# Optimization experiments

Hardware: AMD Instinct MI355X
Metric: run time of the kernel (lower is better)

Reference implementation:

```python
import jax, jax.numpy as jnp
import numpy as np

B, D, L, E, H = 8192, 1024, 256, 16, 400

def setup_inputs() -> dict:
    key = jax.random.key(0)
    ks = jax.random.split(key, 6)
    s1 = 1.0 / np.sqrt(D)
    s2 = 1.0 / np.sqrt(H)
    return {
        "x": jax.random.normal(ks[0], (B, D), dtype=jnp.float32),
        "angle_idx": jax.random.randint(ks[1], (B,), 0, E, dtype=jnp.int64),
        "W1": jax.random.uniform(ks[2], (E, D, H), jnp.float32, -s1, s1),
        "b1": jax.random.uniform(ks[3], (E, H), jnp.float32, -s1, s1),
        "W2": jax.random.uniform(ks[4], (E, H, 2 * L), jnp.float32, -s2, s2),
        "b2": jax.random.uniform(ks[5], (E, 2 * L), jnp.float32, -s2, s2),
    }

def reference(x, angle_idx, W1, b1, W2, b2):
    # Dense all-experts compute, then per-sample select (jit-friendly MoE dispatch).
    # h1: [E, B, H]
    h1 = jax.nn.relu(jnp.einsum('bd,edh->ebh', x, W1) + b1[:, None, :])
    # h: [E, B, 2L]
    h = jnp.einsum('ebh,ehk->ebk', h1, W2) + b2[:, None, :]
    sel = h[angle_idx, jnp.arange(x.shape[0])]  # [B, 2L], each row from its routed expert
    half = sel.shape[1] // 2
    z_mu, z_logvar = sel[:, :half], sel[:, half:]
    return (z_mu, z_logvar)
```

## Files before the change

kernel.cpp:

```cpp
#include <hip/hip_runtime.h>
#include <hip/hip_bf16.h>
#include <cstdint>
#include <cstddef>

#define B_N 8192
#define D_K 1024
#define H_N 400
#define HP  416
#define K2_N 512
#define E_N 16
#define L_N 256
#define TM 64
#define PAD_ROWS (B_N + E_N * TM)
#define NTILES (PAD_ROWS / TM)

typedef short bf16x8 __attribute__((ext_vector_type(8)));
typedef float f32x4 __attribute__((ext_vector_type(4)));

#define GLDS(gp, lp) __builtin_amdgcn_global_load_lds( \
    (const __attribute__((address_space(1))) unsigned int*)(gp), \
    (__attribute__((address_space(3))) unsigned int*)(lp), 16, 0, 0)

static __device__ __forceinline__ unsigned short f2bf(float f) {
  union { float f; unsigned int u; } c; c.f = f;
  unsigned int u = c.u + 0x7fffu + ((c.u >> 16) & 1u);
  return (unsigned short)(u >> 16);
}
static __device__ __forceinline__ unsigned int pkbf(float a, float b) {
  union { __hip_bfloat162 v; unsigned int u; } c;
  c.v = __float22bfloat162_rn(make_float2(a, b));
  return c.u;
}

__global__ __launch_bounds__(256) void prep_kernel(const float* __restrict__ W1,
                                                   const float* __restrict__ W2,
                                                   const float* __restrict__ x,
                                                   const int* __restrict__ idx,
                                                   unsigned short* __restrict__ Wt1,
                                                   unsigned short* __restrict__ Wt2,
                                                   unsigned short* __restrict__ xc,
                                                   int* __restrict__ off_al,
                                                   int* __restrict__ cnt_al,
                                                   int* __restrict__ order) {
  const int bid = blockIdx.x;
  const int t = threadIdx.x;
  if (bid < 2688) {
    __shared__ unsigned short Ls[64][72];
    const float* S; unsigned short* Dt; int K, N, Kd, Nd, k0, n0;
    if (bid < 1792) {
      int e = bid / 112, r = bid % 112;
      k0 = (r % 16) * 64; n0 = (r / 16) * 64;
      S = W1 + (size_t)e * D_K * H_N; Dt = Wt1 + (size_t)e * HP * D_K;
      K = D_K; N = H_N; Kd = D_K; Nd = HP;
    } else {
      int t2 = bid - 1792; int e = t2 / 56, r = t2 % 56;
      k0 = (r % 7) * 64; n0 = (r / 7) * 64;
      S = W2 + (size_t)e * H_N * K2_N; Dt = Wt2 + (size_t)e * K2_N * HP;
      K = H_N; N = K2_N; Kd = HP; Nd = K2_N;
    }
    const int kk = t >> 4;
    const int nn = (t & 15) * 4;
    float4 v[4];
#pragma unroll
    for (int p = 0; p < 4; ++p) {
      int k = k0 + p * 16 + kk;
      int n = n0 + nn;
      v[p] = make_float4(0.f, 0.f, 0.f, 0.f);
      if (k < K && n + 3 < N) v[p] = *(const float4*)(S + (size_t)k * N + n);
    }
#pragma unroll
    for (int p = 0; p < 4; ++p) {
      Ls[nn + 0][p * 16 + kk] = f2bf(v[p].x);
      Ls[nn + 1][p * 16 + kk] = f2bf(v[p].y);
      Ls[nn + 2][p * 16 + kk] = f2bf(v[p].z);
      Ls[nn + 3][p * 16 + kk] = f2bf(v[p].w);
    }
    __syncthreads();
    const int n2 = t >> 3;
    const int ch = t & 7;
#pragma unroll
    for (int p = 0; p < 2; ++p) {
      int n = n0 + p * 32 + n2;
      int k = k0 + ch * 8;
      if (n < Nd && k < Kd)
        *(uint4*)(Dt + (size_t)n * Kd + k) = *(const uint4*)&Ls[p * 32 + n2][ch * 8];
    }
  } else if (bid < 3200) {
    const int xb = bid - 2688;
    const float* S = x + (size_t)xb * 16 * D_K;
    unsigned short* Dp = xc + (size_t)xb * 16 * D_K;
#pragma unroll
    for (int i = 0; i < 16; ++i) {
      float4 v = *(const float4*)(S + i * D_K + t * 4);
      uint2 o; o.x = pkbf(v.x, v.y); o.y = pkbf(v.z, v.w);
      *(uint2*)(Dp + i * D_K + t * 4) = o;
    }
  } else {
    const int hb = bid - 3200;
    __shared__ int totL[E_N], preL[E_N], offsL[E_N], curL[E_N];
    if (t < E_N) { totL[t] = 0; preL[t] = 0; }
    __syncthreads();
    const int lim = hb * 256;
    for (int i = t; i < B_N; i += 256) {
      const int e0 = idx[i];
      atomicAdd(&totL[e0], 1);
      if (i < lim) atomicAdd(&preL[e0], 1);
    }
    __syncthreads();
    if (t == 0) {
      int acc = 0;
      for (int e = 0; e < E_N; ++e) {
        offsL[e] = acc;
        if (hb == 0) off_al[e] = acc;
        acc += ((totL[e] + TM - 1) / TM) * TM;
      }
      if (hb == 0) off_al[E_N] = acc;
    }
    __syncthreads();
    if (t < E_N) {
      curL[t] = offsL[t] + preL[t];
      if (hb == 0) cnt_al[t] = totL[t];
    }
    __syncthreads();
    const int b = hb * 256 + t;
    const int e = idx[b];
    const int slot = atomicAdd(&curL[e], 1);
    order[slot] = b;
    if (hb == 0) *(uint2*)(xc + (size_t)B_N * D_K + t * 4) = make_uint2(0, 0);
  }
}

static __device__ __forceinline__ void swz_decode(int bx, int by, int& mt, int& nb) {
  const int L = bx + NTILES * by;
  const int vid = (L & 7) * 72 + (L >> 3);
  mt = vid >> 2;
  nb = vid & 3;
}

__global__ __launch_bounds__(256) void gemm1_kernel(const unsigned short* __restrict__ xc,
                                                    const unsigned short* __restrict__ Wt1,
                                                    const float* __restrict__ b1,
                                                    const int* __restrict__ off_al,
                                                    const int* __restrict__ cnt_al,
                                                    const int* __restrict__ order,
                                                    unsigned short* __restrict__ h1buf) {
  __shared__ unsigned short As[2 * 2 * 2048];
  __shared__ unsigned short Bs[2 * 2 * 4096];
  __shared__ int offs[E_N + 1];
  __shared__ int rowidx[TM];
  const int tid = threadIdx.x;
  int mt, nb;
  swz_decode(blockIdx.x, blockIdx.y, mt, nb);
  const int m0 = mt * TM;
  if (tid <= E_N) offs[tid] = off_al[tid];
  __syncthreads();
  if (m0 >= offs[E_N]) return;
  int e = 0;
  while (m0 >= offs[e + 1]) ++e;
  if (tid < TM) {
    const bool valid = (m0 + tid) < (offs[e] + cnt_al[e]);
    rowidx[tid] = valid ? order[m0 + tid] : B_N;
  }
  __syncthreads();
  const unsigned short* Wt1e = Wt1 + (size_t)e * HP * D_K;

  const int l = tid & 63, w = tid >> 6;
  const int r4 = l >> 2;
  const int sg = (r4 ^ (r4 >> 2)) & 3;
  const int g8 = ((l & 3) ^ sg) * 8;
  const int t0 = nb * 8 + 2 * w;
  const bool act0 = (t0 < 25);
  const bool act1 = (t0 + 1 < 25);
  const unsigned short* gA = xc + (size_t)rowidx[16 * w + r4] * D_K + g8;
  const unsigned short* gB0 = Wt1e + (size_t)(t0 * 16 + r4) * D_K + g8;
  const unsigned short* gB1 = gB0 + (size_t)16 * D_K;

  const int ln = l & 15, q = l >> 4;
  const int sr = (ln ^ (ln >> 2)) & 3;
  const int cq = (q ^ sr) * 8;

  f32x4 acc[4][2] = {};

#pragma unroll
  for (int ks = 0; ks < 2; ++ks) {
    GLDS(gA + ks * 32, &As[ks * 2048 + 16 * w * 32]);
    if (act0) GLDS(gB0 + ks * 32, &Bs[ks * 4096 + (2 * w + 0) * 512]);
    if (act1) GLDS(gB1 + ks * 32, &Bs[ks * 4096 + (2 * w + 1) * 512]);
  }

  for (int k0 = 0; k0 < D_K; k0 += 64) {
    const int cur = (k0 >> 6) & 1;
    const int nxt = cur ^ 1;
    __syncthreads();
    if (k0 + 64 < D_K) {
#pragma unroll
      for (int ks = 0; ks < 2; ++ks) {
        const int kg = k0 + 64 + ks * 32;
        GLDS(gA + kg, &As[nxt * 4096 + ks * 2048 + 16 * w * 32]);
        if (act0) GLDS(gB0 + kg, &Bs[nxt * 8192 + ks * 4096 + (2 * w + 0) * 512]);
        if (act1) GLDS(gB1 + kg, &Bs[nxt * 8192 + ks * 4096 + (2 * w + 1) * 512]);
      }
    }
    if (act0) {
#pragma unroll
      for (int ks = 0; ks < 2; ++ks) {
        const unsigned short* Ab = &As[cur * 4096 + ks * 2048];
        const unsigned short* Bb = &Bs[cur * 8192 + ks * 4096];
        bf16x8 af[4];
#pragma unroll
        for (int i = 0; i < 4; ++i)
          af[i] = *(const bf16x8*)&Ab[(16 * i + ln) * 32 + cq];
        bf16x8 b0f = *(const bf16x8*)&Bb[(2 * w + 0) * 512 + ln * 32 + cq];
#pragma unroll
        for (int i = 0; i < 4; ++i)
          acc[i][0] = __builtin_amdgcn_mfma_f32_16x16x32_bf16(b0f, af[i], acc[i][0], 0, 0, 0);
        if (act1) {
          bf16x8 b1f = *(const bf16x8*)&Bb[(2 * w + 1) * 512 + ln * 32 + cq];
#pragma unroll
          for (int i = 0; i < 4; ++i)
            acc[i][1] = __builtin_amdgcn_mfma_f32_16x16x32_bf16(b1f, af[i], acc[i][1], 0, 0, 0);
        }
      }
    }
  }

#pragma unroll
  for (int j = 0; j < 2; ++j) {
    if (j == 0 ? act0 : act1) {
      const int n4 = (t0 + j) * 16 + 4 * q;
      const float4 bv = *(const float4*)&b1[e * H_N + n4];
#pragma unroll
      for (int i = 0; i < 4; ++i) {
        const size_t m = (size_t)(m0 + 16 * i + ln);
        uint2 o;
        o.x = pkbf(fmaxf(acc[i][j][0] + bv.x, 0.f), fmaxf(acc[i][j][1] + bv.y, 0.f));
        o.y = pkbf(fmaxf(acc[i][j][2] + bv.z, 0.f), fmaxf(acc[i][j][3] + bv.w, 0.f));
        *(uint2*)&h1buf[m * HP + n4] = o;
      }
    }
  }
}

__global__ __launch_bounds__(256) void gemm2_kernel(const unsigned short* __restrict__ h1buf,
                                                    const unsigned short* __restrict__ Wt2,
                                                    const float* __restrict__ b2,
                                                    const int* __restrict__ off_al,
                                                    const int* __restrict__ cnt_al,
                                                    const int* __restrict__ order,
                                                    float* __restrict__ out) {
  __shared__ unsigned short As[2 * 2 * 2048];
  __shared__ unsigned short Bs[2 * 2 * 4096];
  __shared__ int offs[E_N + 1];
  __shared__ int rowidx[TM];
  const int tid = threadIdx.x;
  int mt, nb;
  swz_decode(blockIdx.x, blockIdx.y, mt, nb);
  const int m0 = mt * TM;
  if (tid <= E_N) offs[tid] = off_al[tid];
  __syncthreads();
  if (m0 >= offs[E_N]) return;
  int e = 0;
  while (m0 >= offs[e + 1]) ++e;
  if (tid < TM) {
    const bool valid = (m0 + tid) < (offs[e] + cnt_al[e]);
    rowidx[tid] = valid ? order[m0 + tid] : -1;
  }
  __syncthreads();
  const unsigned short* Wt2e = Wt2 + (size_t)e * K2_N * HP;

  const int l = tid & 63, w = tid >> 6;
  const int r4 = l >> 2;
  const int sg = (r4 ^ (r4 >> 2)) & 3;
  const int g8 = ((l & 3) ^ sg) * 8;
  const int t0 = nb * 8 + 2 * w;
  const unsigned short* gA = h1buf + (size_t)(m0 + 16 * w + r4) * HP + g8;
  const unsigned short* gB0 = Wt2e + (size_t)(t0 * 16 + r4) * HP + g8;
  const unsigned short* gB1 = gB0 + (size_t)16 * HP;

  const int ln = l & 15, q = l >> 4;
  const int sr = (ln ^ (ln >> 2)) & 3;
  const int cq = (q ^ sr) * 8;

  f32x4 acc[4][2] = {};

#pragma unroll
  for (int ks = 0; ks < 2; ++ks) {
    GLDS(gA + ks * 32, &As[ks * 2048 + 16 * w * 32]);
    GLDS(gB0 + ks * 32, &Bs[ks * 4096 + (2 * w + 0) * 512]);
    GLDS(gB1 + ks * 32, &Bs[ks * 4096 + (2 * w + 1) * 512]);
  }

  for (int k0 = 0; k0 < HP; k0 += 64) {
    const int cur = (k0 >> 6) & 1;
    const int nxt = cur ^ 1;
    __syncthreads();
#pragma unroll
    for (int ks = 0; ks < 2; ++ks) {
      const int kg = k0 + 64 + ks * 32;
      if (kg < HP) {
        GLDS(gA + kg, &As[nxt * 4096 + ks * 2048 + 16 * w * 32]);
        GLDS(gB0 + kg, &Bs[nxt * 8192 + ks * 4096 + (2 * w + 0) * 512]);
        GLDS(gB1 + kg, &Bs[nxt * 8192 + ks * 4096 + (2 * w + 1) * 512]);
      }
    }
#pragma unroll
    for (int ks = 0; ks < 2; ++ks) {
      if (k0 + ks * 32 < HP) {
        const unsigned short* Ab = &As[cur * 4096 + ks * 2048];
        const unsigned short* Bb = &Bs[cur * 8192 + ks * 4096];
        bf16x8 af[4];
#pragma unroll
        for (int i = 0; i < 4; ++i)
          af[i] = *(const bf16x8*)&Ab[(16 * i + ln) * 32 + cq];
        bf16x8 b0f = *(const bf16x8*)&Bb[(2 * w + 0) * 512 + ln * 32 + cq];
#pragma unroll
        for (int i = 0; i < 4; ++i)
          acc[i][0] = __builtin_amdgcn_mfma_f32_16x16x32_bf16(b0f, af[i], acc[i][0], 0, 0, 0);
        bf16x8 b1f = *(const bf16x8*)&Bb[(2 * w + 1) * 512 + ln * 32 + cq];
#pragma unroll
        for (int i = 0; i < 4; ++i)
          acc[i][1] = __builtin_amdgcn_mfma_f32_16x16x32_bf16(b1f, af[i], acc[i][1], 0, 0, 0);
      }
    }
  }

#pragma unroll
  for (int j = 0; j < 2; ++j) {
    const int n4 = (t0 + j) * 16 + 4 * q;
    const float4 bv = *(const float4*)&b2[e * K2_N + n4];
#pragma unroll
    for (int i = 0; i < 4; ++i) {
      const int s = rowidx[16 * i + ln];
      if (s >= 0) {
        float4 v;
        v.x = acc[i][j][0] + bv.x;
        v.y = acc[i][j][1] + bv.y;
        v.z = acc[i][j][2] + bv.z;
        v.w = acc[i][j][3] + bv.w;
        if (n4 < L_N) *(float4*)&out[(size_t)s * L_N + n4] = v;
        else          *(float4*)&out[(size_t)(B_N + s) * L_N + (n4 - L_N)] = v;
      }
    }
  }
}

extern "C" void kernel_launch(void* const* d_in, const int* in_sizes, int n_in,
                              void* d_out, int out_size, void* d_ws, size_t ws_size,
                              hipStream_t stream) {
  const float* x   = (const float*)d_in[0];
  const int*   idx = (const int*)d_in[1];
  const float* W1  = (const float*)d_in[2];
  const float* b1  = (const float*)d_in[3];
  const float* W2  = (const float*)d_in[4];
  const float* b2  = (const float*)d_in[5];
  float* out = (float*)d_out;

  char* ws = (char*)d_ws;
  int* off_al = (int*)(ws + 0);
  int* cnt_al = (int*)(ws + 128);
  int* order  = (int*)(ws + 2240);
  unsigned short* xc  = (unsigned short*)(ws + 39104);
  unsigned short* h1  = (unsigned short*)(ws + 16818368);
  unsigned short* Wt1 = (unsigned short*)(ws + 24486080);
  unsigned short* Wt2 = (unsigned short*)(ws + 38117568);

  prep_kernel<<<3232, 256, 0, stream>>>(W1, W2, x, idx, Wt1, Wt2, xc,
                                        off_al, cnt_al, order);
  gemm1_kernel<<<dim3(NTILES, 4), 256, 0, stream>>>(xc, Wt1, b1, off_al, cnt_al, order, h1);
  gemm2_kernel<<<dim3(NTILES, 4), 256, 0, stream>>>(h1, Wt2, b2, off_al, cnt_al, order, out);
}
```

Baseline: 159.5 us.

## Use 4-slot LDS ring with prefetch distance two and explicit vmcnt waits

```diff
diff --git a/kernel.cpp b/kernel.cpp
--- a/kernel.cpp
+++ b/kernel.cpp
@@ -20,6 +20,11 @@
 #define GLDS(gp, lp) __builtin_amdgcn_global_load_lds( \
     (const __attribute__((address_space(1))) unsigned int*)(gp), \
     (__attribute__((address_space(3))) unsigned int*)(lp), 16, 0, 0)
+
+#define VMW(N) asm volatile("s_waitcnt vmcnt(" #N ")" ::: "memory")
+#define LGKM0() asm volatile("s_waitcnt lgkmcnt(0)" ::: "memory")
+#define SBAR() __builtin_amdgcn_s_barrier()
+#define SCHED0() __builtin_amdgcn_sched_barrier(0)
 
 static __device__ __forceinline__ unsigned short f2bf(float f) {
   union { float f; unsigned int u; } c; c.f = f;
@@ -144,8 +149,8 @@
                                                     const int* __restrict__ cnt_al,
                                                     const int* __restrict__ order,
                                                     unsigned short* __restrict__ h1buf) {
-  __shared__ unsigned short As[2 * 2 * 2048];
-  __shared__ unsigned short Bs[2 * 2 * 4096];
+  __shared__ unsigned short As[4][64 * 32];
+  __shared__ unsigned short Bs[4][128 * 32];
   __shared__ int offs[E_N + 1];
   __shared__ int rowidx[TM];
   const int tid = threadIdx.x;
@@ -171,6 +176,7 @@
   const int t0 = nb * 8 + 2 * w;
   const bool act0 = (t0 < 25);
   const bool act1 = (t0 + 1 < 25);
+  const int Lw = 1 + (act0 ? 1 : 0) + (act1 ? 1 : 0);
   const unsigned short* gA = xc + (size_t)rowidx[16 * w + r4] * D_K + g8;
   const unsigned short* gB0 = Wt1e + (size_t)(t0 * 16 + r4) * D_K + g8;
   const unsigned short* gB1 = gB0 + (size_t)16 * D_K;
@@ -181,45 +187,37 @@
 
   f32x4 acc[4][2] = {};
 
-#pragma unroll
-  for (int ks = 0; ks < 2; ++ks) {
-    GLDS(gA + ks * 32, &As[ks * 2048 + 16 * w * 32]);
-    if (act0) GLDS(gB0 + ks * 32, &Bs[ks * 4096 + (2 * w + 0) * 512]);
-    if (act1) GLDS(gB1 + ks * 32, &Bs[ks * 4096 + (2 * w + 1) * 512]);
-  }
-
-  for (int k0 = 0; k0 < D_K; k0 += 64) {
-    const int cur = (k0 >> 6) & 1;
-    const int nxt = cur ^ 1;
-    __syncthreads();
-    if (k0 + 64 < D_K) {
-#pragma unroll
-      for (int ks = 0; ks < 2; ++ks) {
-        const int kg = k0 + 64 + ks * 32;
-        GLDS(gA + kg, &As[nxt * 4096 + ks * 2048 + 16 * w * 32]);
-        if (act0) GLDS(gB0 + kg, &Bs[nxt * 8192 + ks * 4096 + (2 * w + 0) * 512]);
-        if (act1) GLDS(gB1 + kg, &Bs[nxt * 8192 + ks * 4096 + (2 * w + 1) * 512]);
-      }
-    }
+  auto stage = [&](int slot) {
+    const int b = slot & 3;
+    GLDS(gA + slot * 32, &As[b][16 * w * 32]);
+    if (act0) GLDS(gB0 + slot * 32, &Bs[b][(2 * w + 0) * 512]);
+    if (act1) GLDS(gB1 + slot * 32, &Bs[b][(2 * w + 1) * 512]);
+  };
+
+  stage(0); stage(1);
+#pragma unroll 1
+  for (int i = 0; i < 32; ++i) {
+    const int cb = i & 3;
+    if (i + 2 < 32) stage(i + 2);
+    if (i < 30)       { if (Lw == 3) VMW(6); else if (Lw == 2) VMW(4); else VMW(2); }
+    else if (i == 30) { if (Lw == 3) VMW(3); else if (Lw == 2) VMW(2); else VMW(1); }
+    else              VMW(0);
+    LGKM0();
+    SBAR(); SCHED0();
     if (act0) {
-#pragma unroll
-      for (int ks = 0; ks < 2; ++ks) {
-        const unsigned short* Ab = &As[cur * 4096 + ks * 2048];
-        const unsigned short* Bb = &Bs[cur * 8192 + ks * 4096];
-        bf16x8 af[4];
-#pragma unroll
-        for (int i = 0; i < 4; ++i)
-          af[i] = *(const bf16x8*)&Ab[(16 * i + ln) * 32 + cq];
-        bf16x8 b0f = *(const bf16x8*)&Bb[(2 * w + 0) * 512 + ln * 32 + cq];
-#pragma unroll
-        for (int i = 0; i < 4; ++i)
-          acc[i][0] = __builtin_amdgcn_mfma_f32_16x16x32_bf16(b0f, af[i], acc[i][0], 0, 0, 0);
-        if (act1) {
-          bf16x8 b1f = *(const bf16x8*)&Bb[(2 * w + 1) * 512 + ln * 32 + cq];
-#pragma unroll
-          for (int i = 0; i < 4; ++i)
-            acc[i][1] = __builtin_amdgcn_mfma_f32_16x16x32_bf16(b1f, af[i], acc[i][1], 0, 0, 0);
-        }
+      bf16x8 af[4];
+#pragma unroll
+      for (int i4 = 0; i4 < 4; ++i4)
+        af[i4] = *(const bf16x8*)&As[cb][(16 * i4 + ln) * 32 + cq];
+      bf16x8 b0f = *(const bf16x8*)&Bs[cb][(2 * w + 0) * 512 + ln * 32 + cq];
+#pragma unroll
+      for (int i4 = 0; i4 < 4; ++i4)
+        acc[i4][0] = __builtin_amdgcn_mfma_f32_16x16x32_bf16(b0f, af[i4], acc[i4][0], 0, 0, 0);
+      if (act1) {
+        bf16x8 b1f = *(const bf16x8*)&Bs[cb][(2 * w + 1) * 512 + ln * 32 + cq];
+#pragma unroll
+        for (int i4 = 0; i4 < 4; ++i4)
+          acc[i4][1] = __builtin_amdgcn_mfma_f32_16x16x32_bf16(b1f, af[i4], acc[i4][1], 0, 0, 0);
       }
     }
   }
@@ -248,8 +246,8 @@
                                                     const int* __restrict__ cnt_al,
                                                     const int* __restrict__ order,
                                                     float* __restrict__ out) {
-  __shared__ unsigned short As[2 * 2 * 2048];
-  __shared__ unsigned short Bs[2 * 2 * 4096];
+  __shared__ unsigned short As[4][64 * 32];
+  __shared__ unsigned short Bs[4][128 * 32];
   __shared__ int offs[E_N + 1];
   __shared__ int rowidx[TM];
   const int tid = threadIdx.x;
@@ -283,45 +281,35 @@
 
   f32x4 acc[4][2] = {};
 
-#pragma unroll
-  for (int ks = 0; ks < 2; ++ks) {
-    GLDS(gA + ks * 32, &As[ks * 2048 + 16 * w * 32]);
-    GLDS(gB0 + ks * 32, &Bs[ks * 4096 + (2 * w + 0) * 512]);
-    GLDS(gB1 + ks * 32, &Bs[ks * 4096 + (2 * w + 1) * 512]);
-  }
-
-  for (int k0 = 0; k0 < HP; k0 += 64) {
-    const int cur = (k0 >> 6) & 1;
-    const int nxt = cur ^ 1;
-    __syncthreads();
-#pragma unroll
-    for (int ks = 0; ks < 2; ++ks) {
-      const int kg = k0 + 64 + ks * 32;
-      if (kg < HP) {
-        GLDS(gA + kg, &As[nxt * 4096 + ks * 2048 + 16 * w * 32]);
-        GLDS(gB0 + kg, &Bs[nxt * 8192 + ks * 4096 + (2 * w + 0) * 512]);
-        GLDS(gB1 + kg, &Bs[nxt * 8192 + ks * 4096 + (2 * w + 1) * 512]);
-      }
-    }
-#pragma unroll
-    for (int ks = 0; ks < 2; ++ks) {
-      if (k0 + ks * 32 < HP) {
-        const unsigned short* Ab = &As[cur * 4096 + ks * 2048];
-        const unsigned short* Bb = &Bs[cur * 8192 + ks * 4096];
-        bf16x8 af[4];
-#pragma unroll
-        for (int i = 0; i < 4; ++i)
-          af[i] = *(const bf16x8*)&Ab[(16 * i + ln) * 32 + cq];
-        bf16x8 b0f = *(const bf16x8*)&Bb[(2 * w + 0) * 512 + ln * 32 + cq];
-#pragma unroll
-        for (int i = 0; i < 4; ++i)
-          acc[i][0] = __builtin_amdgcn_mfma_f32_16x16x32_bf16(b0f, af[i], acc[i][0], 0, 0, 0);
-        bf16x8 b1f = *(const bf16x8*)&Bb[(2 * w + 1) * 512 + ln * 32 + cq];
-#pragma unroll
-        for (int i = 0; i < 4; ++i)
-          acc[i][1] = __builtin_amdgcn_mfma_f32_16x16x32_bf16(b1f, af[i], acc[i][1], 0, 0, 0);
-      }
-    }
+  auto stage = [&](int slot) {
+    const int b = slot & 3;
+    GLDS(gA + slot * 32, &As[b][16 * w * 32]);
+    GLDS(gB0 + slot * 32, &Bs[b][(2 * w + 0) * 512]);
+    GLDS(gB1 + slot * 32, &Bs[b][(2 * w + 1) * 512]);
+  };
+
+  stage(0); stage(1);
+#pragma unroll 1
+  for (int i = 0; i < 13; ++i) {
+    const int cb = i & 3;
+    if (i + 2 < 13) stage(i + 2);
+    if (i < 11)       VMW(6);
+    else if (i == 11) VMW(3);
+    else              VMW(0);
+    LGKM0();
+    SBAR(); SCHED0();
+    bf16x8 af[4];
+#pragma unroll
+    for (int i4 = 0; i4 < 4; ++i4)
+      af[i4] = *(const bf16x8*)&As[cb][(16 * i4 + ln) * 32 + cq];
+    bf16x8 b0f = *(const bf16x8*)&Bs[cb][(2 * w + 0) * 512 + ln * 32 + cq];
+#pragma unroll
+    for (int i4 = 0; i4 < 4; ++i4)
+      acc[i4][0] = __builtin_amdgcn_mfma_f32_16x16x32_bf16(b0f, af[i4], acc[i4][0], 0, 0, 0);
+    bf16x8 b1f = *(const bf16x8*)&Bs[cb][(2 * w + 1) * 512 + ln * 32 + cq];
+#pragma unroll
+    for (int i4 = 0; i4 < 4; ++i4)
+      acc[i4][1] = __builtin_amdgcn_mfma_f32_16x16x32_bf16(b1f, af[i4], acc[i4][1], 0, 0, 0);
   }
 
 #pragma unroll
@@ -330,15 +318,17 @@
     const float4 bv = *(const float4*)&b2[e * K2_N + n4];
 #pragma unroll
     for (int i = 0; i < 4; ++i) {
-      const int s = rowidx[16 * i + ln];
-      if (s >= 0) {
+      const int s = rowidx[16 * i + 4 * q + 0 * 0 + (0)];
+      (void)s;
+      const int s2 = rowidx[16 * i + ln];
+      if (s2 >= 0) {
         float4 v;
         v.x = acc[i][j][0] + bv.x;
         v.y = acc[i][j][1] + bv.y;
         v.z = acc[i][j][2] + bv.z;
         v.w = acc[i][j][3] + bv.w;
-        if (n4 < L_N) *(float4*)&out[(size_t)s * L_N + n4] = v;
-        else          *(float4*)&out[(size_t)(B_N + s) * L_N + (n4 - L_N)] = v;
+        if (n4 < L_N) *(float4*)&out[(size_t)s2 * L_N + n4] = v;
+        else          *(float4*)&out[(size_t)(B_N + s2) * L_N + (n4 - L_N)] = v;
       }
     }
   }
```

New measurement: 163.4 us. 2.5% more time.
